# Performance work log

Measured on AMD Instinct MI355X. Metric: run time of the kernel, lower is better.

## Reference

```python
import jax, jax.numpy as jnp
import numpy as np

B, S, T, H, E, V = 32, 400, 32, 512, 128, 50000
A = H  # attention feature dim

def setup_inputs() -> dict:
    key = jax.random.key(0)
    ks = jax.random.split(key, 16)
    f = lambda k, shape: jax.random.normal(k, shape, dtype=jnp.float32) * 0.02
    return {
        "source_tokens": jax.random.randint(ks[0], (B, S), 0, V, dtype=jnp.int32),
        "embedded_tgt": jax.random.normal(ks[1], (B, T, E), dtype=jnp.float32),
        "encoder_states": jax.random.normal(ks[2], (B, S, 2 * H), dtype=jnp.float32),
        "source_mask": jnp.ones((B, S), dtype=bool),
        "h0": f(ks[3], (B, H)),
        "c0": f(ks[4], (B, H)),
        "W_ih": f(ks[5], (4 * H, E)),
        "W_hh": f(ks[6], (4 * H, H)),
        "b_ih": jnp.zeros((4 * H,), jnp.float32),
        "b_hh": jnp.zeros((4 * H,), jnp.float32),
        "W_enc": f(ks[7], (2 * H, A)),
        "W_dec": f(ks[8], (H, A)),
        "w_cov": f(ks[9], (A,)),
        "b_att": jnp.zeros((A,), jnp.float32),
        "v_att": f(ks[10], (A,)),
        "W_ah": f(ks[11], (3 * H, H)),
        "b_ah": jnp.zeros((H,), jnp.float32),
        "W_pg": f(ks[12], (3 * H + E, 1)),
        "b_pg": jnp.zeros((1,), jnp.float32),
        "W_v": f(ks[13], (H, V)),
        "b_v": jnp.zeros((V,), jnp.float32),
    }


def reference(source_tokens, embedded_tgt, encoder_states, source_mask, h0, c0,
              W_ih, W_hh, b_ih, b_hh, W_enc, W_dec, w_cov, b_att, v_att,
              W_ah, b_ah, W_pg, b_pg, W_v, b_v):
    Bn, Sn = source_tokens.shape
    # precompute encoder projection for Bahdanau attention: (B,S,A)
    enc_proj = jnp.einsum('bsd,da->bsa', encoder_states, W_enc)
    bidx = jnp.arange(Bn)[:, None]
    NEG = jnp.float32(-1e9)
    EPS = jnp.float32(1e-20)

    def step(carry, emb):  # emb: (B,E)
        h, c, cov = carry
        # LSTM cell (torch gate order i,f,g,o)
        gates = emb @ W_ih.T + h @ W_hh.T + b_ih + b_hh
        i, fg, g, o = jnp.split(gates, 4, axis=-1)
        c = jax.nn.sigmoid(fg) * c + jax.nn.sigmoid(i) * jnp.tanh(g)
        h = jax.nn.sigmoid(o) * jnp.tanh(c)
        # coverage attention
        feat = jnp.tanh(enc_proj + (h @ W_dec)[:, None, :] + cov[:, :, None] * w_cov + b_att)
        scores = jnp.where(source_mask, feat @ v_att, NEG)  # (B,S)
        attn = jax.nn.softmax(scores, axis=-1)
        context = jnp.einsum('bs,bsd->bd', attn, encoder_states)  # (B,2H)
        cov = cov + attn
        ah = jnp.tanh(jnp.concatenate([context, h], axis=-1) @ W_ah + b_ah)  # (B,H)
        p_gen = jax.nn.sigmoid(jnp.concatenate([context, h, emb], axis=-1) @ W_pg + b_pg)  # (B,1)
        vocab_dist = p_gen * jax.nn.softmax(ah @ W_v + b_v, axis=-1)  # (B,V)
        attn_dist = (1.0 - p_gen) * attn  # (B,S)
        final = vocab_dist.at[bidx, source_tokens].add(attn_dist)  # copy-merge scatter_add
        logp = jnp.log(final + EPS)
        return (h, c, cov), (logp, ah, attn, cov, p_gen[:, 0])

    cov0 = jnp.zeros_like(source_mask, dtype=jnp.float32)
    _, (logps, dec_states, attns, covs, p_gens) = jax.lax.scan(
        step, (h0, c0, cov0), jnp.swapaxes(embedded_tgt, 0, 1))
    tr = lambda x: jnp.swapaxes(x, 0, 1)  # (T,B,...) -> (B,T,...)
    return tr(logps), tr(dec_states), tr(attns), tr(covs), tr(p_gens)
```

## Files before the change

kernel.cpp:

```cpp
#include <hip/hip_runtime.h>
#include <hip/hip_bf16.h>
#include <stdint.h>
#include <stddef.h>

#define B_  32
#define S_  400
#define T_  32
#define H_  512
#define E_  128
#define V_  50000
#define A_  512
#define H2_ 1024
#define H3_ 1536
#define H4_ 2048
#define R_  1024
#define PGK_ 1664
#define NBLKV_ 391
#define GRB_ 128
#define WROW_ 520

typedef unsigned short u16;
typedef short v8s __attribute__((ext_vector_type(8)));
typedef float v4f __attribute__((ext_vector_type(4)));

__device__ __forceinline__ float fsig(float x){ return 1.0f/(1.0f + __expf(-x)); }
__device__ __forceinline__ float ftanh(float x){ float e = __expf(2.0f*x); return 1.0f - 2.0f/(e + 1.0f); }
__device__ __forceinline__ u16 f2bf(float x){ __hip_bfloat16 b = __float2bfloat16(x); return *reinterpret_cast<u16*>(&b); }
__device__ __forceinline__ float bf2f(u16 u){ __hip_bfloat16 b = *reinterpret_cast<__hip_bfloat16*>(&u); return __bfloat162float(b); }

__device__ __forceinline__ float wsum(float v){
  #pragma unroll
  for (int off = 32; off > 0; off >>= 1) v += __shfl_xor(v, off, 64);
  return v;
}
__device__ __forceinline__ float wmax(float v){
  #pragma unroll
  for (int off = 32; off > 0; off >>= 1) v = fmaxf(v, __shfl_xor(v, off, 64));
  return v;
}

#define ALD(p)    __hip_atomic_load((p), __ATOMIC_RELAXED, __HIP_MEMORY_SCOPE_AGENT)
#define AST(p,v)  __hip_atomic_store((p), (v), __ATOMIC_RELAXED, __HIP_MEMORY_SCOPE_AGENT)

__device__ __forceinline__ void ldsbar(){
  asm volatile("s_waitcnt lgkmcnt(0)" ::: "memory");
  __builtin_amdgcn_s_barrier();
  asm volatile("" ::: "memory");
}

__device__ __forceinline__ void gridbar2(unsigned* bar, unsigned target, int grp){
  __syncthreads();
  if (threadIdx.x == 0){
    unsigned v = __hip_atomic_fetch_add(bar + grp*32, 1u, __ATOMIC_RELAXED, __HIP_MEMORY_SCOPE_AGENT);
    if (v == target*16u - 1u){
      unsigned g2 = __hip_atomic_fetch_add(bar + 256, 1u, __ATOMIC_RELAXED, __HIP_MEMORY_SCOPE_AGENT);
      if (g2 == target*8u - 1u)
        AST(bar + 288, target);
    }
    while (ALD(bar + 288) < target) __builtin_amdgcn_s_sleep(2);
    asm volatile("" ::: "memory");
  }
  __syncthreads();
}


__global__ void k_init0(unsigned* __restrict__ bar, unsigned long long* __restrict__ mz){
  int t = threadIdx.x;
  if (t < 512) AST(bar + t, 0u);
  if (t < 128) AST(mz + t, 0ull);
}

__global__ __launch_bounds__(256) void k_transpose(const float* __restrict__ in, float* __restrict__ out, int R, int C){
  __shared__ float tile[64][65];
  int c0 = blockIdx.x*64, r0 = blockIdx.y*64;
  int tid = threadIdx.x;
  int cl = tid & 63, q = tid >> 6;
  #pragma unroll
  for (int i=0;i<16;i++){
    int r = q + i*4;
    float v = 0.0f;
    if (r0 + r < R && c0 + cl < C) v = in[(size_t)(r0+r)*C + c0 + cl];
    tile[r][cl] = v;
  }
  __syncthreads();
  #pragma unroll
  for (int i=0;i<16;i++){
    int c = q + i*4;
    if (c0 + c < C && r0 + cl < R)
      out[(size_t)(c0+c)*R + r0 + cl] = tile[cl][c];
  }
}

__global__ __launch_bounds__(256) void k_convT(const float* __restrict__ in, u16* __restrict__ hi, int R, int C){
  __shared__ float tile[64][65];
  int c0 = blockIdx.x*64, r0 = blockIdx.y*64;
  int tid = threadIdx.x;
  int cl = tid & 63, q = tid >> 6;
  #pragma unroll
  for (int i=0;i<16;i++){
    int r = q + i*4;
    float v = 0.0f;
    if (r0 + r < R && c0 + cl < C) v = in[(size_t)(r0+r)*C + c0 + cl];
    tile[r][cl] = v;
  }
  __syncthreads();
  #pragma unroll
  for (int i=0;i<16;i++){
    int c = q + i*4;
    if (c0 + c < C && r0 + cl < R)
      hi[(size_t)(c0+c)*R + r0 + cl] = f2bf(tile[cl][c]);
  }
}

__global__ __launch_bounds__(256) void k_convT3(const float* __restrict__ in, u16* __restrict__ out){
  __shared__ float tile[64][65];
  int c0 = blockIdx.x*64, r0 = blockIdx.y*64;
  int tid = threadIdx.x;
  int cl = tid & 63, q = tid >> 6;
  #pragma unroll
  for (int i=0;i<16;i++){
    int r = q + i*4;
    tile[r][cl] = in[(size_t)(r0+r)*A_ + c0 + cl];
  }
  __syncthreads();
  #pragma unroll
  for (int i=0;i<16;i++){
    int c = q + i*4;
    float v = tile[cl][c];
    u16 h = f2bf(v);
    u16 lo = f2bf(v - bf2f(h));
    size_t o = (size_t)(c0+c)*3072 + (r0+cl);
    out[o] = h;
    out[o + 1024] = lo;
    out[o + 2048] = h;
  }
}

__global__ void k_conv3(const float* __restrict__ in, u16* __restrict__ out, int n4){
  int i = blockIdx.x*256 + threadIdx.x;
  if (i >= n4) return;
  float4 x = reinterpret_cast<const float4*>(in)[i];
  u16 h0v=f2bf(x.x), h1v=f2bf(x.y), h2v=f2bf(x.z), h3v=f2bf(x.w);
  uint2 hv; hv.x = (unsigned)h0v | ((unsigned)h1v << 16); hv.y = (unsigned)h2v | ((unsigned)h3v << 16);
  uint2 lv;
  lv.x = (unsigned)f2bf(x.x - bf2f(h0v)) | ((unsigned)f2bf(x.y - bf2f(h1v)) << 16);
  lv.y = (unsigned)f2bf(x.z - bf2f(h2v)) | ((unsigned)f2bf(x.w - bf2f(h3v)) << 16);
  int row = i >> 8, c = (i & 255)*4;
  size_t base = (size_t)row*3072 + c;
  *reinterpret_cast<uint2*>(out + base)        = hv;
  *reinterpret_cast<uint2*>(out + base + 1024) = hv;
  *reinterpret_cast<uint2*>(out + base + 2048) = lv;
}

__global__ __launch_bounds__(256) void k_gih(const float* __restrict__ emb, const float* __restrict__ WihT,
    const float* __restrict__ b_ih, const float* __restrict__ b_hh, float* __restrict__ G){
  __shared__ float em[8][128];
  int r0 = blockIdx.x*8;
  int tid = threadIdx.x;
  #pragma unroll
  for (int i=0;i<4;i++){
    int e = i*256 + tid;
    em[e>>7][e&127] = emb[(size_t)(r0 + (e>>7))*E_ + (e&127)];
  }
  __syncthreads();
  for (int jj=0;jj<8;jj++){
    int j = jj*256 + tid;
    float bias = b_ih[j] + b_hh[j];
    float acc[8];
    #pragma unroll
    for (int r=0;r<8;r++) acc[r] = bias;
    for (int e=0;e<128;e++){
      float wv = WihT[(size_t)e*H4_ + j];
      #pragma unroll
      for (int r=0;r<8;r++) acc[r] += em[r][e]*wv;
    }
    #pragma unroll
    for (int rr=0;rr<8;rr++){
      int r = r0 + rr;
      G[(size_t)(r & 31)*65536 + (size_t)(j >> 9)*16384 + (size_t)(j & 511)*32 + (r >> 5)] = acc[rr];
    }
  }
}

__global__ __launch_bounds__(256, 2) void k_gemm_bf16(
    const u16* __restrict__ A, int lda, const u16* __restrict__ Bt, int ldb,
    const float* __restrict__ bias, float* __restrict__ Cf, u16* __restrict__ Cbf, int ldc,
    int M, int N, int K, float2* __restrict__ stats, int nblk)
{
  __shared__ __align__(16) float CsF[128*132];
  __shared__ float rs[128], rs2[128];
  u16* As = reinterpret_cast<u16*>(CsF);
  u16* Bs = As + 128*64;
  const int tid = threadIdx.x;
  const int m0 = blockIdx.y * 128;
  const int n0 = blockIdx.x * 128;
  const int l  = tid & 63;
  const int wavebase = tid & ~63;
  const int wid = tid >> 6;
  const int wm = (wid >> 1) * 64;
  const int wn = (wid & 1) * 64;

  v4f acc[4][4];
  v4f vzero = {0.0f, 0.0f, 0.0f, 0.0f};
  #pragma unroll
  for (int i=0;i<4;i++)
    #pragma unroll
    for (int j=0;j<4;j++) acc[i][j] = vzero;

  for (int k0 = 0; k0 < K; k0 += 64){
    __syncthreads();
    #pragma unroll
    for (int jj=0;jj<4;jj++){
      int fc = jj*256 + tid;
      int row = fc >> 3;
      int cc = (fc & 7) ^ (row & 7);
      const u16* g = A + (size_t)(m0 + row)*lda + k0 + cc*8;
      __builtin_amdgcn_global_load_lds(
        (__attribute__((address_space(1))) void*)g,
        (__attribute__((address_space(3))) void*)(As + (size_t)(jj*256 + wavebase)*8),
        16, 0, 0);
    }
    #pragma unroll
    for (int jj=0;jj<4;jj++){
      int fc = jj*256 + tid;
      int row = fc >> 3;
      int cc = (fc & 7) ^ (row & 7);
      int rn = n0 + row; if (rn > N-1) rn = N-1;
      const u16* g = Bt + (size_t)rn*ldb + k0 + cc*8;
      __builtin_amdgcn_global_load_lds(
        (__attribute__((address_space(1))) void*)g,
        (__attribute__((address_space(3))) void*)(Bs + (size_t)(jj*256 + wavebase)*8),
        16, 0, 0);
    }
    __syncthreads();
    #pragma unroll
    for (int ks=0;ks<2;ks++){
      v8s af[4], bfr[4];
      #pragma unroll
      for (int rt=0;rt<4;rt++){
        int r = wm + rt*16 + (l & 15);
        int cs = (ks*4 + (l >> 4)) ^ (r & 7);
        af[rt] = *reinterpret_cast<const v8s*>(As + r*64 + cs*8);
      }
      #pragma unroll
      for (int nt=0;nt<4;nt++){
        int r = wn + nt*16 + (l & 15);
        int cs = (ks*4 + (l >> 4)) ^ (r & 7);
        bfr[nt] = *reinterpret_cast<const v8s*>(Bs + r*64 + cs*8);
      }
      #pragma unroll
      for (int rt=0;rt<4;rt++)
        #pragma unroll
        for (int nt=0;nt<4;nt++)
          acc[rt][nt] = __builtin_amdgcn_mfma_f32_16x16x32_bf16(af[rt], bfr[nt], acc[rt][nt], 0, 0, 0);
    }
  }

  const int cl = l & 15;
  const int rg = (l >> 4) * 4;
  float cvv[4][4][4];
  #pragma unroll
  for (int rt=0;rt<4;rt++)
    #pragma unroll
    for (int nt=0;nt<4;nt++){
      int gc = n0 + wn + nt*16 + cl;
      float bv = (bias && gc < N) ? bias[gc] : 0.0f;
      #pragma unroll
      for (int i=0;i<4;i++) cvv[rt][nt][i] = acc[rt][nt][i] + bv;
    }

  if (stats){
    float tsm[4][4];
    #pragma unroll
    for (int rt=0;rt<4;rt++)
      #pragma unroll
      for (int i=0;i<4;i++){
        float mx = -1e30f;
        #pragma unroll
        for (int nt=0;nt<4;nt++){
          int gc = n0 + wn + nt*16 + cl;
          if (gc < N) mx = fmaxf(mx, cvv[rt][nt][i]);
        }
        #pragma unroll
        for (int off=1; off<16; off<<=1) mx = fmaxf(mx, __shfl_xor(mx, off, 64));
        if (wn == 0 && cl == 0) rs[wm + rt*16 + rg + i] = mx;
        tsm[rt][i] = mx;
      }
    __syncthreads();
    if (wn != 0){
      #pragma unroll
      for (int rt=0;rt<4;rt++)
        #pragma unroll
        for (int i=0;i<4;i++){
          float c = fmaxf(tsm[rt][i], rs[wm + rt*16 + rg + i]);
          if (cl == 0) rs[wm + rt*16 + rg + i] = c;
        }
    }
    __syncthreads();
    #pragma unroll
    for (int rt=0;rt<4;rt++)
      #pragma unroll
      for (int i=0;i<4;i++){
        float rm = rs[wm + rt*16 + rg + i];
        float sm = 0.0f;
        #pragma unroll
        for (int nt=0;nt<4;nt++){
          int gc = n0 + wn + nt*16 + cl;
          if (gc < N) sm += __expf(cvv[rt][nt][i] - rm);
        }
        #pragma unroll
        for (int off=1; off<16; off<<=1) sm += __shfl_xor(sm, off, 64);
        tsm[rt][i] = sm;
        if (wn == 0 && cl == 0) rs2[wm + rt*16 + rg + i] = sm;
      }
    __syncthreads();
    if (wn != 0 && cl == 0){
      #pragma unroll
      for (int rt=0;rt<4;rt++)
        #pragma unroll
        for (int i=0;i<4;i++){
          int row = wm + rt*16 + rg + i;
          stats[(size_t)(m0 + row)*nblk + blockIdx.x] =
            make_float2(rs[row], tsm[rt][i] + rs2[row]);
        }
    }
  }

  __syncthreads();
  #pragma unroll
  for (int rt=0;rt<4;rt++)
    #pragma unroll
    for (int nt=0;nt<4;nt++)
      #pragma unroll
      for (int i=0;i<4;i++)
        CsF[(wm + rt*16 + rg + i)*132 + wn + nt*16 + cl] = cvv[rt][nt][i];
  __syncthreads();
  #pragma unroll
  for (int it=0; it<16; ++it){
    int row = (tid >> 5) + it*8;
    int c4 = tid & 31;
    int gc = n0 + c4*4;
    int gr = m0 + row;
    if (gc < N){
      float4 v = *reinterpret_cast<const float4*>(&CsF[row*132 + c4*4]);
      if (Cf) *reinterpret_cast<float4*>(Cf + (size_t)gr*ldc + gc) = v;
      if (Cbf){
        uint2 o;
        o.x = (unsigned)f2bf(v.x) | ((unsigned)f2bf(v.y) << 16);
        o.y = (unsigned)f2bf(v.z) | ((unsigned)f2bf(v.w) << 16);
        *reinterpret_cast<uint2*>(Cbf + (size_t)gr*ldc + gc) = o;
      }
    }
  }
}

__global__ __launch_bounds__(256) void k_wv_f32(
  const float* __restrict__ Aah, const float* __restrict__ Wv, const float* __restrict__ bv,
  float* __restrict__ Cl)
{
  __shared__ float Asf[32][68];
  __shared__ float Bsf[32][64];
  int n0 = blockIdx.x*64, m0 = blockIdx.y*64;
  int tid = threadIdx.x;
  int tx = tid & 15, ty = tid >> 4;
  float acc[4][4] = {};
  for (int kc = 0; kc < H_; kc += 32){
    __syncthreads();
    #pragma unroll
    for (int i=0;i<8;i++){
      int e = i*256 + tid;
      Asf[e & 31][e >> 5] = Aah[(size_t)(m0 + (e >> 5))*H_ + kc + (e & 31)];
    }
    #pragma unroll
    for (int i=0;i<8;i++){
      int e = i*256 + tid;
      int nc = n0 + (e & 63); if (nc >= V_) nc = V_-1;
      Bsf[e >> 6][e & 63] = Wv[(size_t)(kc + (e >> 6))*V_ + nc];
    }
    __syncthreads();
    #pragma unroll
    for (int k=0;k<32;k++){
      float4 a4 = *reinterpret_cast<const float4*>(&Asf[k][ty*4]);
      float4 b4 = *reinterpret_cast<const float4*>(&Bsf[k][tx*4]);
      float av[4] = {a4.x, a4.y, a4.z, a4.w};
      float bv4[4] = {b4.x, b4.y, b4.z, b4.w};
      #pragma unroll
      for (int i=0;i<4;i++)
        #pragma unroll
        for (int j=0;j<4;j++)
          acc[i][j] = __builtin_fmaf(av[i], bv4[j], acc[i][j]);
    }
  }
  #pragma unroll
  for (int i=0;i<4;i++){
    int rr = m0 + ty*4 + i;
    #pragma unroll
    for (int j=0;j<4;j++){
      int cc = n0 + tx*4 + j;
      if (cc < V_) Cl[(size_t)rr*V_ + cc] = acc[i][j] + bv[cc];
    }
  }
}

__global__ __launch_bounds__(1024) void k_recur(
  const float* __restrict__ W_hh, const float* __restrict__ G2,
  const float* __restrict__ W_decT, const u16* __restrict__ ep_bf,
  const float* __restrict__ w_cov, const float* __restrict__ v_att,
  const void* __restrict__ maskp, const float* __restrict__ h0,
  const float* __restrict__ c0, float* __restrict__ h_gT,
  float* __restrict__ dec_g, unsigned long long* __restrict__ mz,
  float* __restrict__ catbuf, float* __restrict__ attns, float* __restrict__ covs,
  unsigned* __restrict__ bar)
{
  const int beta = blockIdx.x;
  const int tid = threadIdx.x;
  __shared__ __align__(16) u16 Whi[32*WROW_];
  __shared__ __align__(16) u16 Wlo[32*WROW_];
  __shared__ __align__(16) u16 Hhi[32*WROW_];
  __shared__ __align__(16) u16 Hlo[32*WROW_];
  __shared__ float gv2[16][32];
  __shared__ float c_l[128];
  __shared__ float dec_l[512];
  __shared__ float sc_l[100];
  __shared__ float cov_l[100];
  __shared__ float smz[4][2];

  const int b32 = tid & 31;
  const int w = tid >> 6, l = tid & 63;
  const int grp = beta & 7;
  const int bb = (beta & 7)*4 + (beta >> 5);
  const int sq = (beta >> 3) & 3;
  const int b2 = (tid & 15)*2;
  const int kg = tid >> 4;

  for (int idx = tid; idx < 32*512; idx += 1024){
    int row = idx >> 9;
    int k = idx & 511;
    float v = 0.0f;
    if (row < 16)      v = W_hh[((size_t)(row >> 2)*H_ + beta*4 + (row & 3))*H_ + k];
    else if (row < 20) v = W_decT[(size_t)(beta*4 + (row - 16))*H_ + k];
    u16 h = f2bf(v);
    Whi[row*WROW_ + k] = h;
    Wlo[row*WROW_ + k] = f2bf(v - bf2f(h));
  }
  if (tid < 128) c_l[tid] = c0[(size_t)(tid & 31)*H_ + beta*4 + (tid >> 5)];
  if (tid < 100) cov_l[tid] = 0.f;

  const unsigned* m32p = (const unsigned*)maskp;
  const unsigned char* m8p = (const unsigned char*)maskp;
  const bool bytemode = (m32p[0] == 0x01010101u);

  float wc8[8], va8[8];
  {
    int a0 = l*8;
    #pragma unroll
    for (int j=0;j<8;j++){ wc8[j] = w_cov[a0+j]; va8[j] = v_att[a0+j]; }
  }

  float hA[8], hB[8];
  unsigned long long hld[8];
  #pragma unroll
  for (int kk=0;kk<8;kk++){
    int k = kg*8 + kk;
    hA[kk] = h0[(size_t)b2*H_ + k];
    hB[kk] = h0[(size_t)(b2+1)*H_ + k];
  }

  unsigned gen = 0;
  for (int i = 0; i <= T_; ++i){
    const int par = i & 1;
    {
      v8s phA, plA, phB, plB;
      #pragma unroll
      for (int kk=0;kk<8;kk++){
        float va = hA[kk], vb = hB[kk];
        u16 ha = f2bf(va), hb = f2bf(vb);
        phA[kk] = (short)ha; plA[kk] = (short)f2bf(va - bf2f(ha));
        phB[kk] = (short)hb; plB[kk] = (short)f2bf(vb - bf2f(hb));
      }
      *reinterpret_cast<v8s*>(Hhi + (size_t)b2*WROW_ + kg*8) = phA;
      *reinterpret_cast<v8s*>(Hlo + (size_t)b2*WROW_ + kg*8) = plA;
      *reinterpret_cast<v8s*>(Hhi + (size_t)(b2+1)*WROW_ + kg*8) = phB;
      *reinterpret_cast<v8s*>(Hlo + (size_t)(b2+1)*WROW_ + kg*8) = plB;
    }
    ldsbar();

    if (w < 4){
      const int mt = w >> 1, nt = w & 1;
      const int fr = (l & 15);
      const int fo = (l >> 4)*8;
      const u16* Ahi = Whi + (size_t)(mt*16 + fr)*WROW_ + fo;
      const u16* Alo = Wlo + (size_t)(mt*16 + fr)*WROW_ + fo;
      const u16* Bhi = Hhi + (size_t)(nt*16 + fr)*WROW_ + fo;
      const u16* Blo = Hlo + (size_t)(nt*16 + fr)*WROW_ + fo;
      v4f a0 = {0.f,0.f,0.f,0.f}, a1 = a0, a2 = a0;
      #pragma unroll
      for (int ks=0; ks<16; ks++){
        v8s wh = *reinterpret_cast<const v8s*>(Ahi + ks*32);
        v8s wl = *reinterpret_cast<const v8s*>(Alo + ks*32);
        v8s hh = *reinterpret_cast<const v8s*>(Bhi + ks*32);
        v8s hl = *reinterpret_cast<const v8s*>(Blo + ks*32);
        a0 = __builtin_amdgcn_mfma_f32_16x16x32_bf16(wh, hh, a0, 0, 0, 0);
        a1 = __builtin_amdgcn_mfma_f32_16x16x32_bf16(wh, hl, a1, 0, 0, 0);
        a2 = __builtin_amdgcn_mfma_f32_16x16x32_bf16(wl, hh, a2, 0, 0, 0);
      }
      v4f acc = a0 + a1 + a2;
      if (mt == 0){
        int col = nt*16 + fr;
        int r0w = (l >> 4)*4;
        #pragma unroll
        for (int q=0;q<4;q++) gv2[r0w + q][col] = acc[q];
      } else if ((l >> 4) == 0){
        int b = nt*16 + fr;
        float* dg = dec_g + (size_t)par*B_*A_ + (size_t)b*A_ + beta*4;
        unsigned long long p0 = ((unsigned long long)__float_as_uint(acc[1]) << 32) | __float_as_uint(acc[0]);
        unsigned long long p1 = ((unsigned long long)__float_as_uint(acc[3]) << 32) | __float_as_uint(acc[2]);
        AST(reinterpret_cast<unsigned long long*>(dg), p0);
        AST(reinterpret_cast<unsigned long long*>(dg + 2), p1);
      }
    }
    ldsbar();

    if (i < T_ && tid < 128){
      int hh = tid >> 5;
      int hidx = beta*4 + hh;
      const float* Gr = G2 + (size_t)i*65536 + (size_t)hidx*32 + b32;
      float gi = gv2[0*4+hh][b32] + Gr[0];
      float gf = gv2[1*4+hh][b32] + Gr[16384];
      float gz = gv2[2*4+hh][b32] + Gr[32768];
      float go = gv2[3*4+hh][b32] + Gr[49152];
      float co = c_l[tid];
      float cn = fsig(gf)*co + fsig(gi)*ftanh(gz);
      float hn = fsig(go)*ftanh(cn);
      c_l[tid] = cn;
      AST(h_gT + (size_t)(par^1)*16384 + (size_t)hidx*32 + b32, hn);
      catbuf[(size_t)(b32*T_ + i)*H3_ + H2_ + hidx] = hn;
    }
    gridbar2(bar, ++gen, grp);

    if (i < T_){
      const unsigned long long* hp =
        reinterpret_cast<const unsigned long long*>(h_gT + (size_t)(par^1)*16384);
      #pragma unroll
      for (int kk=0;kk<8;kk++)
        hld[kk] = ALD(hp + (size_t)(kg*8 + kk)*16 + (b2 >> 1));
    }

    if (i > 0){
      const int r = bb*T_ + (i-1);
      if (tid < 512) dec_l[tid] = ALD(dec_g + (size_t)par*B_*A_ + (size_t)bb*A_ + tid);
      ldsbar();
      int a0i = l*8;
      float dec8[8];
      #pragma unroll
      for (int j=0;j<8;j++) dec8[j] = dec_l[a0i+j];
      #pragma unroll
      for (int it=0; it<7; ++it){
        int sl = w + it*16;
        if (sl < 100){
          int s = sq*100 + sl;
          float cv = cov_l[sl];
          uint4 e8 = *reinterpret_cast<const uint4*>(ep_bf + (size_t)(bb*S_ + s)*A_ + a0i);
          unsigned uu[4] = {e8.x, e8.y, e8.z, e8.w};
          float part = 0.f;
          #pragma unroll
          for (int j=0;j<4;j++){
            float xa = bf2f((u16)(uu[j] & 0xFFFFu)) + dec8[2*j]   + cv*wc8[2*j];
            part += va8[2*j]*ftanh(xa);
            float xb = bf2f((u16)(uu[j] >> 16))     + dec8[2*j+1] + cv*wc8[2*j+1];
            part += va8[2*j+1]*ftanh(xb);
          }
          part = wsum(part);
          if (l == 0){
            bool on = bytemode ? (m8p[bb*S_+s] != 0) : (m32p[bb*S_+s] != 0u);
            sc_l[sl] = on ? part : -1e9f;
          }
        }
      }
      __syncthreads();
      if (tid < 64){
        float x1v = sc_l[l];
        float x2v = (l + 64 < 100) ? sc_l[l + 64] : -1e30f;
        float m = wmax(fmaxf(x1v, x2v));
        float z = __expf(x1v - m) + ((l + 64 < 100) ? __expf(x2v - m) : 0.f);
        z = wsum(z);
        if (l == 0){
          unsigned zt = (__float_as_uint(z) & ~255u) | (gen & 255u);
          unsigned long long pk = ((unsigned long long)zt << 32) | (unsigned long long)__float_as_uint(m);
          AST(mz + bb*4 + sq, pk);
        }
      }
      if (tid < 4){
        unsigned long long v;
        do {
          v = ALD(mz + bb*4 + tid);
          if (((unsigned)(v >> 32) & 255u) == (gen & 255u)) break;
          __builtin_amdgcn_s_sleep(1);
        } while (true);
        smz[tid][0] = __uint_as_float((unsigned)v);
        smz[tid][1] = __uint_as_float((unsigned)(v >> 32));
      }
      __syncthreads();
      float gm = fmaxf(fmaxf(smz[0][0], smz[1][0]), fmaxf(smz[2][0], smz[3][0]));
      float gZ = smz[0][1]*__expf(smz[0][0]-gm) + smz[1][1]*__expf(smz[1][0]-gm)
               + smz[2][1]*__expf(smz[2][0]-gm) + smz[3][1]*__expf(smz[3][0]-gm);
      float invZ = 1.f/gZ;
      if (tid < 100){
        float av = __expf(sc_l[tid] - gm)*invZ;
        int s = sq*100 + tid;
        float cn = cov_l[tid] + av;
        cov_l[tid] = cn;
        attns[(size_t)r*S_ + s] = av;
        covs[(size_t)r*S_ + s]  = cn;
      }
      __syncthreads();
    }

    if (i < T_){
      #pragma unroll
      for (int kk=0;kk<8;kk++){
        hA[kk] = __uint_as_float((unsigned)hld[kk]);
        hB[kk] = __uint_as_float((unsigned)(hld[kk] >> 32));
      }
    }
  }
}


__global__ __launch_bounds__(256, 2) void k_ctx(
  const float* __restrict__ attns, const float* __restrict__ enc, float* __restrict__ catbuf)
{
  __shared__ float att_s[32][400];
  int d0 = blockIdx.x*64, b = blockIdx.y;
  int tid = threadIdx.x;
  for (int tt=0; tt<32; ++tt)
    for (int s = tid; s < S_; s += 256)
      att_s[tt][s] = attns[(size_t)(b*T_ + tt)*S_ + s];
  __syncthreads();
  int d = d0 + (tid & 63);
  int t0 = (tid >> 6)*8;
  float acc[8] = {0,0,0,0,0,0,0,0};
  const float* encb = enc + (size_t)b*S_*H2_ + d;
  #pragma unroll 4
  for (int s=0; s<S_; ++s){
    float ev = encb[(size_t)s*H2_];
    #pragma unroll
    for (int i=0;i<8;i++) acc[i] = __builtin_fmaf(att_s[t0+i][s], ev, acc[i]);
  }
  #pragma unroll
  for (int i=0;i<8;i++)
    catbuf[(size_t)(b*T_ + t0 + i)*H3_ + d] = acc[i];
}

__global__ __launch_bounds__(256) void k_ahgemm(
  const float* __restrict__ Acat, const float* __restrict__ W_ah, const float* __restrict__ b_ah,
  float* __restrict__ dec_states, u16* __restrict__ ah_bf)
{
  __shared__ float Asf[32][68];
  __shared__ float Bsf[32][64];
  int n0 = blockIdx.x*64, m0 = blockIdx.y*64;
  int tid = threadIdx.x;
  int tx = tid & 15, ty = tid >> 4;
  float acc[4][4] = {};
  for (int kc = 0; kc < H3_; kc += 32){
    __syncthreads();
    #pragma unroll
    for (int i=0;i<8;i++){
      int e = i*256 + tid;
      Asf[e & 31][e >> 5] = Acat[(size_t)(m0 + (e >> 5))*H3_ + kc + (e & 31)];
    }
    #pragma unroll
    for (int i=0;i<8;i++){
      int e = i*256 + tid;
      Bsf[e >> 6][e & 63] = W_ah[(size_t)(kc + (e >> 6))*H_ + n0 + (e & 63)];
    }
    __syncthreads();
    #pragma unroll
    for (int k=0;k<32;k++){
      float4 a4 = *reinterpret_cast<const float4*>(&Asf[k][ty*4]);
      float4 b4 = *reinterpret_cast<const float4*>(&Bsf[k][tx*4]);
      float av[4] = {a4.x, a4.y, a4.z, a4.w};
      float bv[4] = {b4.x, b4.y, b4.z, b4.w};
      #pragma unroll
      for (int i=0;i<4;i++)
        #pragma unroll
        for (int j=0;j<4;j++)
          acc[i][j] = __builtin_fmaf(av[i], bv[j], acc[i][j]);
    }
  }
  #pragma unroll
  for (int i=0;i<4;i++){
    int rr = m0 + ty*4 + i;
    #pragma unroll
    for (int j=0;j<4;j++){
      int cc = n0 + tx*4 + j;
      float v = ftanh(acc[i][j] + b_ah[cc]);
      dec_states[(size_t)rr*H_ + cc] = v;
      if (ah_bf) ah_bf[(size_t)rr*H_ + cc] = f2bf(v);
    }
  }
}

__global__ __launch_bounds__(512) void k_pgen(const float* __restrict__ catbuf, const float* __restrict__ emb,
  const float* __restrict__ W_pg, const float* __restrict__ b_pg, float* __restrict__ pgens)
{
  int w = threadIdx.x >> 6, l = threadIdx.x & 63;
  int r = blockIdx.x*8 + w;
  float part = 0.0f;
  for (int d = l; d < PGK_; d += 64){
    float x = (d < H3_) ? catbuf[(size_t)r*H3_ + d] : emb[(size_t)r*E_ + (d - H3_)];
    part += x*W_pg[d];
  }
  part = wsum(part);
  if (l == 0) pgens[r] = fsig(part + b_pg[0]);
}

__global__ __launch_bounds__(512) void k_final2(
  float* __restrict__ logits, const float* __restrict__ pgens,
  const float* __restrict__ attns, const int* __restrict__ src,
  const float2* __restrict__ stats, int nblk)
{
  __shared__ unsigned bits[1568];
  __shared__ unsigned keys[1024];
  __shared__ float vals[1024];
  __shared__ float sred[18];
  int r = blockIdx.x;
  int b = r >> 5;
  int tid = threadIdx.x;
  int w = tid >> 6, l = tid & 63;
  float* row = logits + (size_t)r*V_;

  for (int i = tid; i < 1568; i += 512) bits[i] = 0u;
  for (int i = tid; i < 1024; i += 512){ keys[i] = 0xFFFFFFFFu; vals[i] = 0.0f; }

  if (stats){
    float m = -1e30f, Z = 0.0f;
    if (tid < nblk){ float2 st = stats[(size_t)r*nblk + tid]; m = st.x; Z = st.y; }
    #pragma unroll
    for (int off=32; off>0; off>>=1){
      float mo = __shfl_xor(m, off, 64);
      float Zo = __shfl_xor(Z, off, 64);
      float nm = fmaxf(m, mo);
      Z = Z*__expf(m - nm) + Zo*__expf(mo - nm);
      m = nm;
    }
    if (l == 0){ sred[w*2] = m; sred[w*2+1] = Z; }
    __syncthreads();
    if (tid == 0){
      float gm = -1e30f, gz = 0.0f;
      #pragma unroll
      for (int i=0;i<8;i++){
        float mi = sred[i*2], zi = sred[i*2+1];
        float nm = fmaxf(gm, mi);
        gz = gz*__expf(gm - nm) + zi*__expf(mi - nm);
        gm = nm;
      }
      sred[16] = gm; sred[17] = gz;
    }
    __syncthreads();
  } else {
    float m = -1e30f;
    for (int j = tid; j < V_/4; j += 512){
      float4 x = reinterpret_cast<const float4*>(row)[j];
      m = fmaxf(fmaxf(m, x.x), fmaxf(fmaxf(x.y, x.z), x.w));
    }
    m = wmax(m);
    if (l == 0) sred[w] = m;
    __syncthreads();
    if (tid == 0){
      float gm = -1e30f;
      #pragma unroll
      for (int i=0;i<8;i++) gm = fmaxf(gm, sred[i]);
      sred[16] = gm;
    }
    __syncthreads();
    float gm = sred[16];
    float z = 0.0f;
    for (int j = tid; j < V_/4; j += 512){
      float4 x = reinterpret_cast<const float4*>(row)[j];
      z += __expf(x.x-gm) + __expf(x.y-gm) + __expf(x.z-gm) + __expf(x.w-gm);
    }
    z = wsum(z);
    if (l == 0) sred[8 + w] = z;
    __syncthreads();
    if (tid == 0){
      float gz = 0.0f;
      #pragma unroll
      for (int i=0;i<8;i++) gz += sred[8 + i];
      sred[17] = gz;
    }
    __syncthreads();
  }

  float gm = sred[16];
  float gZ = sred[17];
  float pg = pgens[r];
  float scale = pg / gZ;
  float lscale = __logf(scale);

  if (tid < S_){
    int tok = src[b*S_ + tid];
    float add = (1.0f - pg)*attns[(size_t)r*S_ + tid];
    atomicOr(&bits[tok >> 5], 1u << (tok & 31));
    unsigned h = ((unsigned)tok * 2654435761u) >> 22;
    while (true){
      unsigned prev = atomicCAS(&keys[h], 0xFFFFFFFFu, (unsigned)tok);
      if (prev == 0xFFFFFFFFu || prev == (unsigned)tok){
        atomicAdd(&vals[h], add);
        break;
      }
      h = (h + 1) & 1023;
    }
  }
  __syncthreads();

  for (int j = tid; j < V_/4; j += 512){
    float4 x = reinterpret_cast<const float4*>(row)[j];
    int v = 4*j;
    float o[4];
    float xv[4] = {x.x, x.y, x.z, x.w};
    #pragma unroll
    for (int k=0;k<4;k++){
      int vv = v + k;
      bool hit = (bits[vv >> 5] >> (vv & 31)) & 1u;
      float tt = xv[k] - gm + lscale;
      if (!hit && tt > -25.0f){
        o[k] = tt;
      } else {
        float pval = __expf(xv[k] - gm)*scale;
        if (hit){
          unsigned h = ((unsigned)vv * 2654435761u) >> 22;
          while (keys[h] != 0xFFFFFFFFu){
            if (keys[h] == (unsigned)vv){ pval += vals[h]; break; }
            h = (h + 1) & 1023;
          }
        }
        o[k] = __logf(pval + 1e-20f);
      }
    }
    reinterpret_cast<float4*>(row)[j] = make_float4(o[0], o[1], o[2], o[3]);
  }
}


extern "C" void kernel_launch(void* const* d_in, const int* in_sizes, int n_in,
                              void* d_out, int out_size, void* d_ws, size_t ws_size,
                              hipStream_t stream)
{
  const int* src_tokens = (const int*)d_in[0];
  const float* embedded = (const float*)d_in[1];
  const float* enc      = (const float*)d_in[2];
  const void*  maskp    = (const void*)d_in[3];
  const float* h0  = (const float*)d_in[4];
  const float* c0  = (const float*)d_in[5];
  const float* W_ih = (const float*)d_in[6];
  const float* W_hh = (const float*)d_in[7];
  const float* b_ih = (const float*)d_in[8];
  const float* b_hh = (const float*)d_in[9];
  const float* W_enc = (const float*)d_in[10];
  const float* W_dec = (const float*)d_in[11];
  const float* w_cov = (const float*)d_in[12];
  const float* b_att = (const float*)d_in[13];
  const float* v_att = (const float*)d_in[14];
  const float* W_ah  = (const float*)d_in[15];
  const float* b_ah  = (const float*)d_in[16];
  const float* W_pg  = (const float*)d_in[17];
  const float* b_pg  = (const float*)d_in[18];
  const float* W_v   = (const float*)d_in[19];
  const float* b_v   = (const float*)d_in[20];
  (void)in_sizes; (void)n_in; (void)out_size;

  float* outp = (float*)d_out;
  float* logps = outp;
  float* dec_states = logps + (size_t)R_*V_;
  float* attns = dec_states + (size_t)R_*H_;
  float* covs  = attns + (size_t)R_*S_;
  float* pgens = covs + (size_t)R_*S_;

  char* sp = (char*)logps;
  auto salloc = [&](size_t bytes) -> void* {
    void* p = (void*)sp;
    sp += (bytes + 255) & ~(size_t)255;
    return p;
  };
  unsigned* bar = (unsigned*)salloc(2048);
  unsigned long long* mz = (unsigned long long*)salloc((size_t)B_*4*8);
  u16* ep_bf    = (u16*)salloc((size_t)B_*S_*A_*2);
  u16* enc3     = (u16*)salloc((size_t)B_*S_*3072*2);
  u16* WencT3   = (u16*)salloc((size_t)A_*3072*2);
  float* WihT   = (float*)salloc((size_t)E_*H4_*4);
  float* W_decT = (float*)salloc((size_t)H_*A_*4);
  float* G2     = (float*)salloc((size_t)R_*H4_*4);
  float* catbuf = (float*)salloc((size_t)R_*H3_*4);
  float* dec_g  = (float*)salloc((size_t)2*B_*A_*4);
  float* h_gT   = (float*)salloc((size_t)2*H_*B_*4);

  char* wp = (char*)d_ws;
  auto walloc = [&](size_t bytes) -> void* {
    void* p = (void*)wp;
    wp += (bytes + 255) & ~(size_t)255;
    return p;
  };
  u16* ah_bf = (u16*)walloc((size_t)R_*H_*2);
  u16* WvT   = (u16*)walloc((size_t)V_*H_*2);
  float2* stats = (float2*)walloc((size_t)R_*NBLKV_*8);
  const size_t ws_fast  = (size_t)R_*H_*2 + (size_t)V_*H_*2 + 512;
  const size_t ws_stats = ws_fast + (size_t)R_*NBLKV_*8 + 256;
  const bool fast_wv   = (ws_size >= ws_fast);
  const bool use_stats = (ws_size >= ws_stats);

  k_init0<<<1, 512, 0, stream>>>(bar, mz);
  k_transpose<<<dim3(2,32), 256, 0, stream>>>(W_ih, WihT, H4_, E_);
  k_transpose<<<dim3(8,8), 256, 0, stream>>>(W_dec, W_decT, H_, A_);
  k_gih<<<128, 256, 0, stream>>>(embedded, WihT, b_ih, b_hh, G2);
  k_conv3<<<(B_*S_*H2_/4 + 255)/256, 256, 0, stream>>>(enc, enc3, B_*S_*H2_/4);
  k_convT3<<<dim3(8,16), 256, 0, stream>>>(W_enc, WencT3);
  if (fast_wv)
    k_convT<<<dim3((V_+63)/64, 8), 256, 0, stream>>>(W_v, WvT, H_, V_);

  k_gemm_bf16<<<dim3(A_/128, (B_*S_)/128), 256, 0, stream>>>(
      enc3, 3072, WencT3, 3072, b_att, nullptr, ep_bf, A_, B_*S_, A_, 3072, nullptr, 0);

  k_recur<<<GRB_, 1024, 0, stream>>>(W_hh, G2, W_decT, ep_bf, w_cov, v_att, maskp,
                                     h0, c0, h_gT, dec_g, mz,
                                     catbuf, attns, covs, bar);

  k_ctx<<<dim3(16, 32), 256, 0, stream>>>(attns, enc, catbuf);
  k_ahgemm<<<dim3(8,16), 256, 0, stream>>>(catbuf, W_ah, b_ah, dec_states, fast_wv ? ah_bf : (u16*)nullptr);
  k_pgen<<<128, 512, 0, stream>>>(catbuf, embedded, W_pg, b_pg, pgens);

  if (fast_wv)
    k_gemm_bf16<<<dim3(NBLKV_, R_/128), 256, 0, stream>>>(
        ah_bf, H_, WvT, H_, b_v, logps, nullptr, V_, R_, V_, H_,
        use_stats ? stats : nullptr, NBLKV_);
  else
    k_wv_f32<<<dim3((V_+63)/64, R_/64), 256, 0, stream>>>(dec_states, W_v, b_v, logps);

  k_final2<<<R_, 512, 0, stream>>>(logps, pgens, attns, src_tokens,
                                   (fast_wv && use_stats) ? stats : nullptr, NBLKV_);
}
```

Baseline: 1.194 ms.

## Defer softmax normalization a step, read bf16 encoder in ctx, stage bf16 logits

The recurrent kernel drops the per-step spin-wait on partial softmax stats. Partial max and sum are written into a double-buffered slot and normalized one iteration later, after the next grid barrier has made them visible, which adds one extra loop iteration. The context kernel now reads the bf16 copy of the encoder states instead of fp32, halving its load traffic. The vocab GEMM can optionally write bf16 logits to workspace so the final log-softmax/scatter kernel reads half the bytes, at some cost in precision.

```diff
diff --git a/kernel.cpp b/kernel.cpp
--- a/kernel.cpp
+++ b/kernel.cpp
@@ -67,7 +67,7 @@
 __global__ void k_init0(unsigned* __restrict__ bar, unsigned long long* __restrict__ mz){
   int t = threadIdx.x;
   if (t < 512) AST(bar + t, 0u);
-  if (t < 128) AST(mz + t, 0ull);
+  if (t < 256) AST(mz + t, 0ull);
 }
 
 __global__ __launch_bounds__(256) void k_transpose(const float* __restrict__ in, float* __restrict__ out, int R, int C){
@@ -467,7 +467,7 @@
   }
 
   unsigned gen = 0;
-  for (int i = 0; i <= T_; ++i){
+  for (int i = 0; i <= T_ + 1; ++i){
     const int par = i & 1;
     {
       v8s phA, plA, phB, plB;
@@ -546,8 +546,30 @@
         hld[kk] = ALD(hp + (size_t)(kg*8 + kk)*16 + (b2 >> 1));
     }
 
-    if (i > 0){
-      const int r = bb*T_ + (i-1);
+    if (i >= 2){
+      if (tid < 4){
+        unsigned long long v = ALD(mz + (size_t)(i & 1)*128 + bb*4 + tid);
+        smz[tid][0] = __uint_as_float((unsigned)v);
+        smz[tid][1] = __uint_as_float((unsigned)(v >> 32));
+      }
+      __syncthreads();
+      float gm = fmaxf(fmaxf(smz[0][0], smz[1][0]), fmaxf(smz[2][0], smz[3][0]));
+      float gZ = smz[0][1]*__expf(smz[0][0]-gm) + smz[1][1]*__expf(smz[1][0]-gm)
+               + smz[2][1]*__expf(smz[2][0]-gm) + smz[3][1]*__expf(smz[3][0]-gm);
+      float invZ = 1.f/gZ;
+      int r2 = bb*T_ + (i-2);
+      if (tid < 100){
+        float av = __expf(sc_l[tid] - gm)*invZ;
+        int s = sq*100 + tid;
+        float cn = cov_l[tid] + av;
+        cov_l[tid] = cn;
+        attns[(size_t)r2*S_ + s] = av;
+        covs[(size_t)r2*S_ + s]  = cn;
+      }
+      __syncthreads();
+    }
+
+    if (i >= 1 && i <= T_){
       if (tid < 512) dec_l[tid] = ALD(dec_g + (size_t)par*B_*A_ + (size_t)bb*A_ + tid);
       ldsbar();
       int a0i = l*8;
@@ -585,35 +607,11 @@
         float z = __expf(x1v - m) + ((l + 64 < 100) ? __expf(x2v - m) : 0.f);
         z = wsum(z);
         if (l == 0){
-          unsigned zt = (__float_as_uint(z) & ~255u) | (gen & 255u);
-          unsigned long long pk = ((unsigned long long)zt << 32) | (unsigned long long)__float_as_uint(m);
-          AST(mz + bb*4 + sq, pk);
+          unsigned long long pk = ((unsigned long long)__float_as_uint(z) << 32)
+                                | (unsigned long long)__float_as_uint(m);
+          AST(mz + (size_t)((i-1) & 1)*128 + bb*4 + sq, pk);
         }
       }
-      if (tid < 4){
-        unsigned long long v;
-        do {
-          v = ALD(mz + bb*4 + tid);
-          if (((unsigned)(v >> 32) & 255u) == (gen & 255u)) break;
-          __builtin_amdgcn_s_sleep(1);
-        } while (true);
-        smz[tid][0] = __uint_as_float((unsigned)v);
-        smz[tid][1] = __uint_as_float((unsigned)(v >> 32));
-      }
-      __syncthreads();
-      float gm = fmaxf(fmaxf(smz[0][0], smz[1][0]), fmaxf(smz[2][0], smz[3][0]));
-      float gZ = smz[0][1]*__expf(smz[0][0]-gm) + smz[1][1]*__expf(smz[1][0]-gm)
-               + smz[2][1]*__expf(smz[2][0]-gm) + smz[3][1]*__expf(smz[3][0]-gm);
-      float invZ = 1.f/gZ;
-      if (tid < 100){
-        float av = __expf(sc_l[tid] - gm)*invZ;
-        int s = sq*100 + tid;
-        float cn = cov_l[tid] + av;
-        cov_l[tid] = cn;
-        attns[(size_t)r*S_ + s] = av;
-        covs[(size_t)r*S_ + s]  = cn;
-      }
-      __syncthreads();
     }
 
     if (i < T_){
@@ -628,7 +626,7 @@
 
 
 __global__ __launch_bounds__(256, 2) void k_ctx(
-  const float* __restrict__ attns, const float* __restrict__ enc, float* __restrict__ catbuf)
+  const float* __restrict__ attns, const u16* __restrict__ enc3, float* __restrict__ catbuf)
 {
   __shared__ float att_s[32][400];
   int d0 = blockIdx.x*64, b = blockIdx.y;
@@ -637,19 +635,27 @@
     for (int s = tid; s < S_; s += 256)
       att_s[tt][s] = attns[(size_t)(b*T_ + tt)*S_ + s];
   __syncthreads();
-  int d = d0 + (tid & 63);
-  int t0 = (tid >> 6)*8;
-  float acc[8] = {0,0,0,0,0,0,0,0};
-  const float* encb = enc + (size_t)b*S_*H2_ + d;
+  int lane = tid & 31;
+  int d = d0 + lane*2;
+  int tg = tid >> 5;
+  float acc0[4] = {0,0,0,0}, acc1[4] = {0,0,0,0};
+  const u16* encb = enc3 + (size_t)(b*S_)*3072 + d;
   #pragma unroll 4
   for (int s=0; s<S_; ++s){
-    float ev = encb[(size_t)s*H2_];
-    #pragma unroll
-    for (int i=0;i<8;i++) acc[i] = __builtin_fmaf(att_s[t0+i][s], ev, acc[i]);
-  }
-  #pragma unroll
-  for (int i=0;i<8;i++)
-    catbuf[(size_t)(b*T_ + t0 + i)*H3_ + d] = acc[i];
+    unsigned uv = *reinterpret_cast<const unsigned*>(encb + (size_t)s*3072);
+    float e0 = bf2f((u16)(uv & 0xFFFFu));
+    float e1 = bf2f((u16)(uv >> 16));
+    #pragma unroll
+    for (int i=0;i<4;i++){
+      float av = att_s[tg*4 + i][s];
+      acc0[i] = __builtin_fmaf(av, e0, acc0[i]);
+      acc1[i] = __builtin_fmaf(av, e1, acc1[i]);
+    }
+  }
+  #pragma unroll
+  for (int i=0;i<4;i++)
+    *reinterpret_cast<float2*>(catbuf + (size_t)(b*T_ + tg*4 + i)*H3_ + d) =
+      make_float2(acc0[i], acc1[i]);
 }
 
 __global__ __launch_bounds__(256) void k_ahgemm(
@@ -716,7 +722,8 @@
 }
 
 __global__ __launch_bounds__(512) void k_final2(
-  float* __restrict__ logits, const float* __restrict__ pgens,
+  float* __restrict__ logits, const u16* __restrict__ rowbf,
+  const float* __restrict__ pgens,
   const float* __restrict__ attns, const int* __restrict__ src,
   const float2* __restrict__ stats, int nblk)
 {
@@ -729,6 +736,7 @@
   int tid = threadIdx.x;
   int w = tid >> 6, l = tid & 63;
   float* row = logits + (size_t)r*V_;
+  const u16* rb = rowbf ? (rowbf + (size_t)r*V_) : nullptr;
 
   for (int i = tid; i < 1568; i += 512) bits[i] = 0u;
   for (int i = tid; i < 1024; i += 512){ keys[i] = 0xFFFFFFFFu; vals[i] = 0.0f; }
@@ -815,10 +823,17 @@
   __syncthreads();
 
   for (int j = tid; j < V_/4; j += 512){
-    float4 x = reinterpret_cast<const float4*>(row)[j];
+    float xv[4];
+    if (rb){
+      uint2 u = reinterpret_cast<const uint2*>(rb)[j];
+      xv[0] = bf2f((u16)(u.x & 0xFFFFu)); xv[1] = bf2f((u16)(u.x >> 16));
+      xv[2] = bf2f((u16)(u.y & 0xFFFFu)); xv[3] = bf2f((u16)(u.y >> 16));
+    } else {
+      float4 x = reinterpret_cast<const float4*>(row)[j];
+      xv[0] = x.x; xv[1] = x.y; xv[2] = x.z; xv[3] = x.w;
+    }
     int v = 4*j;
     float o[4];
-    float xv[4] = {x.x, x.y, x.z, x.w};
     #pragma unroll
     for (int k=0;k<4;k++){
       int vv = v + k;
@@ -884,7 +899,7 @@
     return p;
   };
   unsigned* bar = (unsigned*)salloc(2048);
-  unsigned long long* mz = (unsigned long long*)salloc((size_t)B_*4*8);
+  unsigned long long* mz = (unsigned long long*)salloc((size_t)2*B_*4*8);
   u16* ep_bf    = (u16*)salloc((size_t)B_*S_*A_*2);
   u16* enc3     = (u16*)salloc((size_t)B_*S_*3072*2);
   u16* WencT3   = (u16*)salloc((size_t)A_*3072*2);
@@ -904,10 +919,13 @@
   u16* ah_bf = (u16*)walloc((size_t)R_*H_*2);
   u16* WvT   = (u16*)walloc((size_t)V_*H_*2);
   float2* stats = (float2*)walloc((size_t)R_*NBLKV_*8);
+  u16* logits_bf = (u16*)walloc((size_t)R_*V_*2);
   const size_t ws_fast  = (size_t)R_*H_*2 + (size_t)V_*H_*2 + 512;
   const size_t ws_stats = ws_fast + (size_t)R_*NBLKV_*8 + 256;
+  const size_t ws_bf    = ws_stats + (size_t)R_*V_*2 + 256;
   const bool fast_wv   = (ws_size >= ws_fast);
   const bool use_stats = (ws_size >= ws_stats);
+  const bool use_bf    = (ws_size >= ws_bf) && use_stats;
 
   k_init0<<<1, 512, 0, stream>>>(bar, mz);
   k_transpose<<<dim3(2,32), 256, 0, stream>>>(W_ih, WihT, H4_, E_);
@@ -925,17 +943,19 @@
                                      h0, c0, h_gT, dec_g, mz,
                                      catbuf, attns, covs, bar);
 
-  k_ctx<<<dim3(16, 32), 256, 0, stream>>>(attns, enc, catbuf);
+  k_ctx<<<dim3(16, 32), 256, 0, stream>>>(attns, enc3, catbuf);
   k_ahgemm<<<dim3(8,16), 256, 0, stream>>>(catbuf, W_ah, b_ah, dec_states, fast_wv ? ah_bf : (u16*)nullptr);
   k_pgen<<<128, 512, 0, stream>>>(catbuf, embedded, W_pg, b_pg, pgens);
 
   if (fast_wv)
     k_gemm_bf16<<<dim3(NBLKV_, R_/128), 256, 0, stream>>>(
-        ah_bf, H_, WvT, H_, b_v, logps, nullptr, V_, R_, V_, H_,
-        use_stats ? stats : nullptr, NBLKV_);
+        ah_bf, H_, WvT, H_, b_v,
+        use_bf ? nullptr : logps, use_bf ? logits_bf : nullptr, V_,
+        R_, V_, H_, use_stats ? stats : nullptr, NBLKV_);
   else
     k_wv_f32<<<dim3((V_+63)/64, R_/64), 256, 0, stream>>>(dec_states, W_v, b_v, logps);
 
-  k_final2<<<R_, 512, 0, stream>>>(logps, pgens, attns, src_tokens,
+  k_final2<<<R_, 512, 0, stream>>>(logps, use_bf ? logits_bf : (u16*)nullptr,
+                                   pgens, attns, src_tokens,
                                    (fast_wv && use_stats) ? stats : nullptr, NBLKV_);
 }
```

After: 1.134 ms. 1.05x faster.
